# Optimization experiments

Measured on AMD Instinct MI355X. Metric: run time of the kernel, lower is better.

The kernel has to match this reference:

```python
import jax, jax.numpy as jnp
import numpy as np

B, T, E, D = 8, 2048, 1024, 128


def setup_inputs() -> dict:
    key = jax.random.key(0)
    k1, k2, k3, k4 = jax.random.split(key, 4)
    x = jax.random.normal(k1, (B, T, E), dtype=jnp.float32)
    wq = jax.random.normal(k2, (E, D), dtype=jnp.float32) * (E ** -0.5)
    wk = jax.random.normal(k3, (E, D), dtype=jnp.float32) * (E ** -0.5)
    wv = jax.random.normal(k4, (E, D), dtype=jnp.float32) * (E ** -0.5)
    return {"x": x, "wq": wq, "wk": wk, "wv": wv}


def reference(x, wq, wk, wv):
    # Projections (bias-free Linear): [B,T,E] @ [E,D] -> [B,T,D]
    q = x @ wq
    k = x @ wk
    v = x @ wv
    d = k.shape[-1]
    # Faithful to source: scores / d**(-0.5) == scores * sqrt(d)
    scores = jnp.einsum('btd,bsd->bts', q, k) * (d ** 0.5)
    causal = jnp.tril(jnp.ones((x.shape[1], x.shape[1]), dtype=bool))
    scores = jnp.where(causal, scores, -jnp.inf)
    weights = jax.nn.softmax(scores, axis=-1)  # dropout omitted (eval mode)
    return jnp.einsum('bts,bsd->btd', weights, v)
```

## Files before the change

kernel.cpp:

```cpp
#include <hip/hip_runtime.h>


#define NB 8
#define NT 2048
#define NE 1024
#define ND 128

typedef unsigned short U16;
typedef unsigned int U32;
typedef __attribute__((ext_vector_type(8))) short vbf8;
typedef __attribute__((ext_vector_type(4))) float vf4;

__device__ __forceinline__ U16 f2bf(float f) {
  U32 u = __builtin_bit_cast(U32, f);
  u += 0x7fffu + ((u >> 16) & 1u);
  return (U16)(u >> 16);
}
__device__ __forceinline__ float bf2f(U16 h) {
  U32 u = ((U32)h) << 16;
  return __builtin_bit_cast(float, u);
}
__device__ __forceinline__ void gl_lds16(const void* g, void* l) {
  __builtin_amdgcn_global_load_lds((__attribute__((address_space(1))) void*)g,
                                   (__attribute__((address_space(3))) void*)l, 16, 0, 0);
}

__global__ void wsplit_kernel(const float* __restrict__ wq, const float* __restrict__ wk,
                              const float* __restrict__ wv, U16* __restrict__ wth,
                              U16* __restrict__ wtl) {
  int id = blockIdx.x * 256 + threadIdx.x;
  if (id >= 384 * 1024) return;
  int n = id >> 10, e = id & 1023;
  float v;
  if (n < 128)      v = wq[e * 128 + n] * 11.313708498984761f;
  else if (n < 256) v = wk[e * 128 + (n - 128)];
  else              v = wv[e * 128 + (n - 256)];
  U16 h = f2bf(v);
  wth[id] = h;
  wtl[id] = f2bf(v - bf2f(h));
}

__global__ __launch_bounds__(256, 3) void qkv_kernel(
    const float* __restrict__ x, const U16* __restrict__ wth, const U16* __restrict__ wtl,
    U16* __restrict__ qfh, U16* __restrict__ qfl, U16* __restrict__ kfh,
    U16* __restrict__ kfl, U16* __restrict__ vf) {
  __shared__ __align__(16) char smem[49152];
  char* Ah = smem;
  char* Al = smem + 8192;
  char* Bh = smem + 16384;
  char* Bl = smem + 32768;

  const int tid = threadIdx.x;
  const int w = tid >> 6, lane = tid & 63;
  const int fr = lane & 15, fq = lane >> 4;
  const int m0 = blockIdx.x * 64;
  const int nt = blockIdx.y;
  const U16* bh_src = wth + nt * (128 * 1024);
  const U16* bl_src = wtl + nt * (128 * 1024);

  const vf4 vzero = {0.f, 0.f, 0.f, 0.f};
  vf4 acc[2][4];
#pragma unroll
  for (int i = 0; i < 2; ++i)
#pragma unroll
    for (int j = 0; j < 4; ++j) acc[i][j] = vzero;

  const int wm = (w >> 1) * 32, wn = (w & 1) * 64;
  const int arow = tid >> 2, ag = tid & 3;

  for (int k0 = 0; k0 < 1024; k0 += 64) {
#pragma unroll
    for (int p = 0; p < 4; ++p) {
      const int g = p * 256 + tid;
      const int row = g >> 3, c = g & 7;
      const int sc = c ^ (row & 7);
      const int ldsb = (p * 256 + w * 64) * 16;
      gl_lds16(bh_src + row * 1024 + k0 + sc * 8, Bh + ldsb);
      if (nt < 2) gl_lds16(bl_src + row * 1024 + k0 + sc * 8, Bl + ldsb);
    }
    {
      const float* s = x + (size_t)(m0 + arow) * 1024 + k0 + ag * 8;
      float v0[8], v1[8];
      ((float4*)v0)[0] = *(const float4*)(s);
      ((float4*)v0)[1] = *(const float4*)(s + 4);
      ((float4*)v1)[0] = *(const float4*)(s + 32);
      ((float4*)v1)[1] = *(const float4*)(s + 36);
      vbf8 h0, l0, h1, l1;
#pragma unroll
      for (int i = 0; i < 8; ++i) {
        U16 a = f2bf(v0[i]);
        h0[i] = (short)a; l0[i] = (short)f2bf(v0[i] - bf2f(a));
        U16 b = f2bf(v1[i]);
        h1[i] = (short)b; l1[i] = (short)f2bf(v1[i] - bf2f(b));
      }
      const int sw = arow & 7;
      *(vbf8*)(Ah + arow * 128 + ((ag ^ sw) << 4))       = h0;
      *(vbf8*)(Ah + arow * 128 + (((ag + 4) ^ sw) << 4)) = h1;
      if (nt < 2) {
        *(vbf8*)(Al + arow * 128 + ((ag ^ sw) << 4))       = l0;
        *(vbf8*)(Al + arow * 128 + (((ag + 4) ^ sw) << 4)) = l1;
      }
    }
    __syncthreads();

    if (nt < 2) {
#pragma unroll
      for (int kc = 0; kc < 2; ++kc) {
        vbf8 a_h[2], a_l[2], b_h[4], b_l[4];
#pragma unroll
        for (int i = 0; i < 2; ++i) {
          const int row = wm + i * 16 + fr;
          const int off = row * 128 + (((kc * 4 + fq) ^ (row & 7)) << 4);
          a_h[i] = *(const vbf8*)(Ah + off);
          a_l[i] = *(const vbf8*)(Al + off);
        }
#pragma unroll
        for (int j = 0; j < 4; ++j) {
          const int row = wn + j * 16 + fr;
          const int off = row * 128 + (((kc * 4 + fq) ^ (row & 7)) << 4);
          b_h[j] = *(const vbf8*)(Bh + off);
          b_l[j] = *(const vbf8*)(Bl + off);
        }
#pragma unroll
        for (int i = 0; i < 2; ++i)
#pragma unroll
          for (int j = 0; j < 4; ++j) {
            acc[i][j] = __builtin_amdgcn_mfma_f32_16x16x32_bf16(a_h[i], b_h[j], acc[i][j], 0, 0, 0);
            acc[i][j] = __builtin_amdgcn_mfma_f32_16x16x32_bf16(a_h[i], b_l[j], acc[i][j], 0, 0, 0);
            acc[i][j] = __builtin_amdgcn_mfma_f32_16x16x32_bf16(a_l[i], b_h[j], acc[i][j], 0, 0, 0);
          }
      }
    } else {
#pragma unroll
      for (int kc = 0; kc < 2; ++kc) {
        vbf8 a_h[2], b_h[4];
#pragma unroll
        for (int i = 0; i < 2; ++i) {
          const int row = wm + i * 16 + fr;
          a_h[i] = *(const vbf8*)(Ah + row * 128 + (((kc * 4 + fq) ^ (row & 7)) << 4));
        }
#pragma unroll
        for (int j = 0; j < 4; ++j) {
          const int row = wn + j * 16 + fr;
          b_h[j] = *(const vbf8*)(Bh + row * 128 + (((kc * 4 + fq) ^ (row & 7)) << 4));
        }
#pragma unroll
        for (int i = 0; i < 2; ++i)
#pragma unroll
          for (int j = 0; j < 4; ++j)
            acc[i][j] = __builtin_amdgcn_mfma_f32_16x16x32_bf16(a_h[i], b_h[j], acc[i][j], 0, 0, 0);
      }
    }
    __syncthreads();
  }

  const int b = m0 >> 11;
  if (nt < 2) {
    U16* tlh = (U16*)smem;
    U16* tll = (U16*)(smem + 16896);
#pragma unroll
    for (int i = 0; i < 2; ++i)
#pragma unroll
      for (int j = 0; j < 4; ++j)
#pragma unroll
        for (int r = 0; r < 4; ++r) {
          const int ml = wm + i * 16 + fq * 4 + r;
          const int col = wn + j * 16 + fr;
          const float val = acc[i][j][r];
          const U16 h = f2bf(val);
          tlh[ml * 132 + col] = h;
          tll[ml * 132 + col] = f2bf(val - bf2f(h));
        }
    __syncthreads();
    U16* dh = (nt == 0) ? qfh : kfh;
    U16* dl = (nt == 0) ? qfl : kfl;
    const int g0 = (m0 & 2047) >> 4;
#pragma unroll
    for (int p = 0; p < 4; ++p) {
      const int idx = p * 256 + tid;
      const int gl = idx >> 8, kc = (idx >> 6) & 3, ln = idx & 63;
      const int row = gl * 16 + (ln & 15);
      const int colc = kc * 32 + (ln >> 4) * 8;
      const size_t o = (((size_t)b * 128 + g0 + gl) * 4 + kc) * 512 + ln * 8;
      *(vbf8*)(dh + o) = *(const vbf8*)(tlh + row * 132 + colc);
      *(vbf8*)(dl + o) = *(const vbf8*)(tll + row * 132 + colc);
    }
  } else {
    U16* tl = (U16*)smem;
#pragma unroll
    for (int i = 0; i < 2; ++i)
#pragma unroll
      for (int j = 0; j < 4; ++j)
#pragma unroll
        for (int r = 0; r < 4; ++r) {
          const int ml = wm + i * 16 + fq * 4 + r;
          const int col = wn + j * 16 + fr;
          tl[col * 68 + ml] = f2bf(acc[i][j][r]);
        }
    __syncthreads();
    const int sc0 = (m0 & 2047) >> 5;
#pragma unroll
    for (int p = 0; p < 4; ++p) {
      const int idx = p * 256 + tid;
      const int df = idx >> 7, sc = (idx >> 6) & 1, ln = idx & 63;
      const int d = df * 16 + (ln & 15);
      const int sl = sc * 32 + (ln >> 4) * 8;
      const size_t o = (((size_t)b * 8 + df) * 64 + (sc0 + sc)) * 512 + ln * 8;
      *(vbf8*)(vf + o) = *(const vbf8*)(tl + d * 68 + sl);
    }
  }
}

__global__ __launch_bounds__(256, 3) void flash_kernel(
    const U16* __restrict__ qfh, const U16* __restrict__ qfl,
    const U16* __restrict__ kfh, const U16* __restrict__ kfl,
    const U16* __restrict__ vf, float* __restrict__ out) {
  __shared__ __align__(16) char smem[25088];

  const int tid = threadIdx.x;
  const int w = tid >> 6, lane = tid & 63;
  const int fr = lane & 15, fq = lane >> 4;
  const int sq = w;
  const int bid = blockIdx.x;
  const int bb = bid & 7;
  const int jj = bid >> 3;
  const int g = (jj < 64) ? (127 - jj) : (jj - 64);
  const int q0g = g * 16;

  vbf8 q_h[4], q_l[4];
  {
    const U16* qb = qfh + ((size_t)bb * 128 + g) * 2048 + lane * 8;
    const U16* qlb = qfl + ((size_t)bb * 128 + g) * 2048 + lane * 8;
#pragma unroll
    for (int kc = 0; kc < 4; ++kc) {
      q_h[kc] = *(const vbf8*)(qb + kc * 512);
      q_l[kc] = *(const vbf8*)(qlb + kc * 512);
    }
  }

  const U16* khp = kfh + (size_t)bb * 262144 + (size_t)(sq * 2) * 2048 + lane * 8;
  const U16* klp = kfl + (size_t)bb * 262144 + (size_t)(sq * 2) * 2048 + lane * 8;
  const U16* vfp = vf + (size_t)bb * 262144 + (size_t)sq * 512 + lane * 8;
  U16* pw = (U16*)(smem + w * 1280);

  const vf4 vzero = {0.f, 0.f, 0.f, 0.f};
  vf4 oacc[8];
#pragma unroll
  for (int i = 0; i < 8; ++i) oacc[i] = vzero;
  float m_r[4], l_r[4];
#pragma unroll
  for (int r = 0; r < 4; ++r) { m_r[r] = -__builtin_inff(); l_r[r] = 0.f; }

  const int lim = q0g + 15 - sq * 32;
  const int ntw = (lim >= 0) ? ((lim >> 7) + 1) : 0;

  for (int T = 0; T < ntw; ++T) {
    vbf8 vreg[8];
#pragma unroll
    for (int df = 0; df < 8; ++df) vreg[df] = *(const vbf8*)(vfp + df * 32768);

    vf4 sacc[2] = {vzero, vzero};
    __builtin_amdgcn_s_setprio(1);
#pragma unroll
    for (int sf2 = 0; sf2 < 2; ++sf2) {
#pragma unroll
      for (int kc = 0; kc < 4; ++kc) {
        const vbf8 kh_r = *(const vbf8*)(khp + sf2 * 2048 + kc * 512);
        const vbf8 kl_r = *(const vbf8*)(klp + sf2 * 2048 + kc * 512);
        sacc[sf2] = __builtin_amdgcn_mfma_f32_16x16x32_bf16(q_h[kc], kh_r, sacc[sf2], 0, 0, 0);
        sacc[sf2] = __builtin_amdgcn_mfma_f32_16x16x32_bf16(q_h[kc], kl_r, sacc[sf2], 0, 0, 0);
        sacc[sf2] = __builtin_amdgcn_mfma_f32_16x16x32_bf16(q_l[kc], kh_r, sacc[sf2], 0, 0, 0);
      }
    }
    __builtin_amdgcn_s_setprio(0);

    if (T == ntw - 1) {
#pragma unroll
      for (int sf2 = 0; sf2 < 2; ++sf2) {
        const int s_g = T * 128 + sq * 32 + sf2 * 16 + fr;
#pragma unroll
        for (int r = 0; r < 4; ++r)
          if (s_g > q0g + fq * 4 + r) sacc[sf2][r] = -__builtin_inff();
      }
    }

    float tmax[4];
#pragma unroll
    for (int r = 0; r < 4; ++r) tmax[r] = fmaxf(sacc[0][r], sacc[1][r]);
#pragma unroll
    for (int off = 1; off < 16; off <<= 1)
#pragma unroll
      for (int r = 0; r < 4; ++r) tmax[r] = fmaxf(tmax[r], __shfl_xor(tmax[r], off, 64));

    float alpha[4], mne[4];
#pragma unroll
    for (int r = 0; r < 4; ++r) {
      const float mn = fmaxf(m_r[r], tmax[r]);
      mne[r] = (mn == -__builtin_inff()) ? 0.f : mn;
      alpha[r] = __expf(m_r[r] - mne[r]);
      m_r[r] = mn;
    }

    float psum[4];
    U16 pb[2][4];
#pragma unroll
    for (int sf2 = 0; sf2 < 2; ++sf2)
#pragma unroll
      for (int r = 0; r < 4; ++r) {
        const float pv = __expf(sacc[sf2][r] - mne[r]);
        psum[r] = (sf2 == 0) ? pv : (psum[r] + pv);
        pb[sf2][r] = f2bf(pv);
      }
#pragma unroll
    for (int off = 1; off < 16; off <<= 1)
#pragma unroll
      for (int r = 0; r < 4; ++r) psum[r] += __shfl_xor(psum[r], off, 64);
#pragma unroll
    for (int r = 0; r < 4; ++r) l_r[r] = l_r[r] * alpha[r] + psum[r];
#pragma unroll
    for (int i = 0; i < 8; ++i)
#pragma unroll
      for (int r = 0; r < 4; ++r) oacc[i][r] *= alpha[r];

#pragma unroll
    for (int sf2 = 0; sf2 < 2; ++sf2)
#pragma unroll
      for (int r = 0; r < 4; ++r) pw[(fq * 4 + r) * 40 + sf2 * 16 + fr] = pb[sf2][r];
    asm volatile("s_waitcnt lgkmcnt(0)" ::: "memory");
    const vbf8 pf = *(const vbf8*)(pw + fr * 40 + fq * 8);

    __builtin_amdgcn_s_setprio(1);
#pragma unroll
    for (int df = 0; df < 8; ++df)
      oacc[df] = __builtin_amdgcn_mfma_f32_16x16x32_bf16(pf, vreg[df], oacc[df], 0, 0, 0);
    __builtin_amdgcn_s_setprio(0);

    khp += 16384; klp += 16384; vfp += 2048;
  }

  __syncthreads();
  float* O_d = (float*)smem;
  float* m_s = (float*)(smem + 24576);
  float* l_s = (float*)(smem + 24832);
  if (sq > 0) {
#pragma unroll
    for (int i = 0; i < 8; ++i)
#pragma unroll
      for (int r = 0; r < 4; ++r)
        O_d[((sq - 1) * 16 + fq * 4 + r) * 128 + i * 16 + fr] = oacc[i][r];
  }
  if (fr == 0) {
#pragma unroll
    for (int r = 0; r < 4; ++r) {
      m_s[sq * 16 + fq * 4 + r] = m_r[r];
      l_s[sq * 16 + fq * 4 + r] = l_r[r];
    }
  }
  __syncthreads();
  if (sq == 0) {
#pragma unroll
    for (int r = 0; r < 4; ++r) {
      const int row = fq * 4 + r;
      float mv[4];
      float M = -__builtin_inff();
#pragma unroll
      for (int p = 0; p < 4; ++p) {
        mv[p] = m_s[p * 16 + row];
        M = fmaxf(M, mv[p]);
      }
      float wgt[4], denom = 0.f;
#pragma unroll
      for (int p = 0; p < 4; ++p) {
        wgt[p] = __expf(mv[p] - M);
        denom += wgt[p] * l_s[p * 16 + row];
      }
      const float inv = 1.f / denom;
#pragma unroll
      for (int i = 0; i < 8; ++i) {
        float o = wgt[0] * oacc[i][r];
#pragma unroll
        for (int p = 1; p < 4; ++p)
          o += wgt[p] * O_d[((p - 1) * 16 + row) * 128 + i * 16 + fr];
        out[(size_t)(bb * 2048 + q0g + row) * 128 + i * 16 + fr] = o * inv;
      }
    }
  }
}

extern "C" void kernel_launch(void* const* d_in, const int* in_sizes, int n_in, void* d_out,
                              int out_size, void* d_ws, size_t ws_size, hipStream_t stream) {
  const float* x = (const float*)d_in[0];
  const float* wq = (const float*)d_in[1];
  const float* wk = (const float*)d_in[2];
  const float* wv = (const float*)d_in[3];
  char* ws = (char*)d_ws;
  U16* wth = (U16*)(ws);
  U16* wtl = (U16*)(ws + 786432);
  U16* qfh = (U16*)(ws + 1572864);
  U16* qfl = (U16*)(ws + 5767168);
  U16* kfh = (U16*)(ws + 9961472);
  U16* kfl = (U16*)(ws + 14155776);
  U16* vfr = (U16*)(ws + 18350080);
  float* out = (float*)d_out;

  wsplit_kernel<<<dim3(1536), dim3(256), 0, stream>>>(wq, wk, wv, wth, wtl);
  qkv_kernel<<<dim3(256, 3), dim3(256), 0, stream>>>(x, wth, wtl, qfh, qfl, kfh, kfl, vfr);
  flash_kernel<<<dim3(1024), dim3(256), 0, stream>>>(qfh, qfl, kfh, kfl, vfr, out);
}
```

Baseline: 105.3 us.

## Widen per-wave key tile to 64, use exp2 with folded log2e, skip rescale

```diff
diff --git a/kernel.cpp b/kernel.cpp
--- a/kernel.cpp
+++ b/kernel.cpp
@@ -10,6 +10,8 @@
 typedef unsigned int U32;
 typedef __attribute__((ext_vector_type(8))) short vbf8;
 typedef __attribute__((ext_vector_type(4))) float vf4;
+
+#define EXP2F(x) __builtin_amdgcn_exp2f(x)
 
 __device__ __forceinline__ U16 f2bf(float f) {
   U32 u = __builtin_bit_cast(U32, f);
@@ -32,7 +34,7 @@
   if (id >= 384 * 1024) return;
   int n = id >> 10, e = id & 1023;
   float v;
-  if (n < 128)      v = wq[e * 128 + n] * 11.313708498984761f;
+  if (n < 128)      v = wq[e * 128 + n] * 16.322231701033217f;
   else if (n < 256) v = wk[e * 128 + (n - 128)];
   else              v = wv[e * 128 + (n - 256)];
   U16 h = f2bf(v);
@@ -238,10 +240,10 @@
     }
   }
 
-  const U16* khp = kfh + (size_t)bb * 262144 + (size_t)(sq * 2) * 2048 + lane * 8;
-  const U16* klp = kfl + (size_t)bb * 262144 + (size_t)(sq * 2) * 2048 + lane * 8;
-  const U16* vfp = vf + (size_t)bb * 262144 + (size_t)sq * 512 + lane * 8;
-  U16* pw = (U16*)(smem + w * 1280);
+  const U16* khp = kfh + (size_t)bb * 262144 + (size_t)(sq * 4) * 2048 + lane * 8;
+  const U16* klp = kfl + (size_t)bb * 262144 + (size_t)(sq * 4) * 2048 + lane * 8;
+  const U16* vfp = vf + (size_t)bb * 262144 + (size_t)(sq * 2) * 512 + lane * 8;
+  U16* pw = (U16*)(smem + w * 2304);
 
   const vf4 vzero = {0.f, 0.f, 0.f, 0.f};
   vf4 oacc[8];
@@ -251,91 +253,104 @@
 #pragma unroll
   for (int r = 0; r < 4; ++r) { m_r[r] = -__builtin_inff(); l_r[r] = 0.f; }
 
-  const int lim = q0g + 15 - sq * 32;
-  const int ntw = (lim >= 0) ? ((lim >> 7) + 1) : 0;
+  const int lim = q0g + 15 - sq * 64;
+  const int ntw = (lim >= 0) ? ((lim >> 8) + 1) : 0;
 
   for (int T = 0; T < ntw; ++T) {
-    vbf8 vreg[8];
-#pragma unroll
-    for (int df = 0; df < 8; ++df) vreg[df] = *(const vbf8*)(vfp + df * 32768);
-
-    vf4 sacc[2] = {vzero, vzero};
+    vf4 sacc[4] = {vzero, vzero, vzero, vzero};
     __builtin_amdgcn_s_setprio(1);
 #pragma unroll
-    for (int sf2 = 0; sf2 < 2; ++sf2) {
+    for (int sf = 0; sf < 4; ++sf) {
 #pragma unroll
       for (int kc = 0; kc < 4; ++kc) {
-        const vbf8 kh_r = *(const vbf8*)(khp + sf2 * 2048 + kc * 512);
-        const vbf8 kl_r = *(const vbf8*)(klp + sf2 * 2048 + kc * 512);
-        sacc[sf2] = __builtin_amdgcn_mfma_f32_16x16x32_bf16(q_h[kc], kh_r, sacc[sf2], 0, 0, 0);
-        sacc[sf2] = __builtin_amdgcn_mfma_f32_16x16x32_bf16(q_h[kc], kl_r, sacc[sf2], 0, 0, 0);
-        sacc[sf2] = __builtin_amdgcn_mfma_f32_16x16x32_bf16(q_l[kc], kh_r, sacc[sf2], 0, 0, 0);
+        const vbf8 kh_r = *(const vbf8*)(khp + sf * 2048 + kc * 512);
+        const vbf8 kl_r = *(const vbf8*)(klp + sf * 2048 + kc * 512);
+        sacc[sf] = __builtin_amdgcn_mfma_f32_16x16x32_bf16(q_h[kc], kh_r, sacc[sf], 0, 0, 0);
+        sacc[sf] = __builtin_amdgcn_mfma_f32_16x16x32_bf16(q_h[kc], kl_r, sacc[sf], 0, 0, 0);
+        sacc[sf] = __builtin_amdgcn_mfma_f32_16x16x32_bf16(q_l[kc], kh_r, sacc[sf], 0, 0, 0);
       }
     }
     __builtin_amdgcn_s_setprio(0);
 
     if (T == ntw - 1) {
 #pragma unroll
-      for (int sf2 = 0; sf2 < 2; ++sf2) {
-        const int s_g = T * 128 + sq * 32 + sf2 * 16 + fr;
+      for (int sf = 0; sf < 4; ++sf) {
+        const int s_g = T * 256 + sq * 64 + sf * 16 + fr;
 #pragma unroll
         for (int r = 0; r < 4; ++r)
-          if (s_g > q0g + fq * 4 + r) sacc[sf2][r] = -__builtin_inff();
+          if (s_g > q0g + fq * 4 + r) sacc[sf][r] = -__builtin_inff();
       }
     }
 
     float tmax[4];
 #pragma unroll
-    for (int r = 0; r < 4; ++r) tmax[r] = fmaxf(sacc[0][r], sacc[1][r]);
+    for (int r = 0; r < 4; ++r)
+      tmax[r] = fmaxf(fmaxf(sacc[0][r], sacc[1][r]), fmaxf(sacc[2][r], sacc[3][r]));
 #pragma unroll
     for (int off = 1; off < 16; off <<= 1)
 #pragma unroll
       for (int r = 0; r < 4; ++r) tmax[r] = fmaxf(tmax[r], __shfl_xor(tmax[r], off, 64));
 
-    float alpha[4], mne[4];
+    vbf8 vreg[8][2];
+#pragma unroll
+    for (int df = 0; df < 8; ++df) {
+      vreg[df][0] = *(const vbf8*)(vfp + df * 32768);
+      vreg[df][1] = *(const vbf8*)(vfp + df * 32768 + 512);
+    }
+
+    bool need = false;
+    float mne[4];
 #pragma unroll
     for (int r = 0; r < 4; ++r) {
+      need |= (tmax[r] > m_r[r]);
       const float mn = fmaxf(m_r[r], tmax[r]);
       mne[r] = (mn == -__builtin_inff()) ? 0.f : mn;
-      alpha[r] = __expf(m_r[r] - mne[r]);
-      m_r[r] = mn;
+    }
+    if (__any(need)) {
+#pragma unroll
+      for (int r = 0; r < 4; ++r) {
+        const float alpha = EXP2F(m_r[r] - mne[r]);
+        l_r[r] *= alpha;
+        m_r[r] = fmaxf(m_r[r], tmax[r]);
+#pragma unroll
+        for (int i = 0; i < 8; ++i) oacc[i][r] *= alpha;
+      }
     }
 
     float psum[4];
-    U16 pb[2][4];
-#pragma unroll
-    for (int sf2 = 0; sf2 < 2; ++sf2)
+    U16 pb[4][4];
+#pragma unroll
+    for (int sf = 0; sf < 4; ++sf)
 #pragma unroll
       for (int r = 0; r < 4; ++r) {
-        const float pv = __expf(sacc[sf2][r] - mne[r]);
-        psum[r] = (sf2 == 0) ? pv : (psum[r] + pv);
-        pb[sf2][r] = f2bf(pv);
+        const float pv = EXP2F(sacc[sf][r] - mne[r]);
+        psum[r] = (sf == 0) ? pv : (psum[r] + pv);
+        pb[sf][r] = f2bf(pv);
       }
 #pragma unroll
     for (int off = 1; off < 16; off <<= 1)
 #pragma unroll
       for (int r = 0; r < 4; ++r) psum[r] += __shfl_xor(psum[r], off, 64);
 #pragma unroll
-    for (int r = 0; r < 4; ++r) l_r[r] = l_r[r] * alpha[r] + psum[r];
-#pragma unroll
-    for (int i = 0; i < 8; ++i)
-#pragma unroll
-      for (int r = 0; r < 4; ++r) oacc[i][r] *= alpha[r];
-
-#pragma unroll
-    for (int sf2 = 0; sf2 < 2; ++sf2)
-#pragma unroll
-      for (int r = 0; r < 4; ++r) pw[(fq * 4 + r) * 40 + sf2 * 16 + fr] = pb[sf2][r];
+    for (int r = 0; r < 4; ++r) l_r[r] += psum[r];
+
+#pragma unroll
+    for (int sf = 0; sf < 4; ++sf)
+#pragma unroll
+      for (int r = 0; r < 4; ++r) pw[(fq * 4 + r) * 72 + sf * 16 + fr] = pb[sf][r];
     asm volatile("s_waitcnt lgkmcnt(0)" ::: "memory");
-    const vbf8 pf = *(const vbf8*)(pw + fr * 40 + fq * 8);
+    const vbf8 pf0 = *(const vbf8*)(pw + fr * 72 + fq * 8);
+    const vbf8 pf1 = *(const vbf8*)(pw + fr * 72 + 32 + fq * 8);
 
     __builtin_amdgcn_s_setprio(1);
 #pragma unroll
-    for (int df = 0; df < 8; ++df)
-      oacc[df] = __builtin_amdgcn_mfma_f32_16x16x32_bf16(pf, vreg[df], oacc[df], 0, 0, 0);
+    for (int df = 0; df < 8; ++df) {
+      oacc[df] = __builtin_amdgcn_mfma_f32_16x16x32_bf16(pf0, vreg[df][0], oacc[df], 0, 0, 0);
+      oacc[df] = __builtin_amdgcn_mfma_f32_16x16x32_bf16(pf1, vreg[df][1], oacc[df], 0, 0, 0);
+    }
     __builtin_amdgcn_s_setprio(0);
 
-    khp += 16384; klp += 16384; vfp += 2048;
+    khp += 32768; klp += 32768; vfp += 4096;
   }
 
   __syncthreads();
@@ -371,7 +386,7 @@
       float wgt[4], denom = 0.f;
 #pragma unroll
       for (int p = 0; p < 4; ++p) {
-        wgt[p] = __expf(mv[p] - M);
+        wgt[p] = EXP2F(mv[p] - M);
         denom += wgt[p] * l_s[p * 16 + row];
       }
       const float inv = 1.f / denom;
```

Measured after the change: 94.07 us. -10.7%, faster.
